# Kernel optimization log

Hardware: AMD Instinct MI355X
Metric: run time of the kernel (lower is better)

The kernel has to match this reference:

```python
import jax, jax.numpy as jnp
import numpy as np

B, N, K = 2, 16384, 16
C_IN, C_OUT, SHARE = 64, 64, 8
ATTN = C_OUT // SHARE  # 8
EPS = 1e-5


def bn(x, gamma, beta):
    # BatchNorm2d_P: normalize over (B, N, K) per channel, training-mode batch stats
    m = jnp.mean(x, axis=(0, 1, 2), keepdims=True)
    v = jnp.var(x, axis=(0, 1, 2), keepdims=True)  # biased variance
    return (x - m) * jax.lax.rsqrt(v + EPS) * gamma + beta


def gather(points, idx):
    # points: (B, N, C), idx: (B, N, K) -> (B, N, K, C)
    b, n, k = idx.shape
    flat = idx.reshape(b, n * k)
    out = jnp.take_along_axis(points, flat[:, :, None], axis=1)
    return out.reshape(b, n, k, points.shape[-1])


def setup_inputs() -> dict:
    key = jax.random.key(0)
    ks = jax.random.split(key, 16)
    w = lambda k_, shp: (jax.random.normal(k_, shp, dtype=jnp.float32) * 0.02)
    inp = {
        "xyz": jax.random.normal(ks[0], (B, N, 3), dtype=jnp.float32),
        "features": jax.random.normal(ks[1], (B, N, C_IN), dtype=jnp.float32),
        "knn_idx": jax.random.randint(ks[2], (B, N, K), 0, N),
        "Wq": w(ks[3], (C_IN, C_OUT)), "bq": jnp.zeros((C_OUT,), jnp.float32),
        "Wk": w(ks[4], (C_IN, C_OUT)), "bk": jnp.zeros((C_OUT,), jnp.float32),
        "Wv": w(ks[5], (C_IN, C_OUT)), "bv": jnp.zeros((C_OUT,), jnp.float32),
        "Wd1": w(ks[6], (3, 3)), "bd1": jnp.zeros((3,), jnp.float32),
        "gamma_d": jnp.ones((3,), jnp.float32), "beta_d": jnp.zeros((3,), jnp.float32),
        "Wd2": w(ks[7], (3, C_OUT)), "bd2": jnp.zeros((C_OUT,), jnp.float32),
        "gamma_g1": jnp.ones((C_OUT,), jnp.float32), "beta_g1": jnp.zeros((C_OUT,), jnp.float32),
        "Wg1": w(ks[8], (C_OUT, ATTN)), "bg1": jnp.zeros((ATTN,), jnp.float32),
        "gamma_g2": jnp.ones((ATTN,), jnp.float32), "beta_g2": jnp.zeros((ATTN,), jnp.float32),
        "Wg2": w(ks[9], (ATTN, ATTN)), "bg2": jnp.zeros((ATTN,), jnp.float32),
    }
    return inp


def reference(xyz, features, knn_idx, Wq, bq, Wk, bk, Wv, bv,
              Wd1, bd1, gamma_d, beta_d, Wd2, bd2,
              gamma_g1, beta_g1, Wg1, bg1, gamma_g2, beta_g2, Wg2, bg2):
    q = features @ Wq + bq                       # (B,N,C_OUT)
    k = gather(features @ Wk + bk, knn_idx)      # (B,N,K,C_OUT)
    v = gather(features @ Wv + bv, knn_idx)      # (B,N,K,C_OUT)
    knn_xyz = gather(xyz, knn_idx)               # (B,N,K,3)
    rel = xyz[:, :, None, :] - knn_xyz           # (B,N,K,3)
    # fc_delta: Linear(3,3) -> BN -> ReLU -> Linear(3,C_OUT)
    pos_enc = jax.nn.relu(bn(rel @ Wd1 + bd1, gamma_d, beta_d)) @ Wd2 + bd2  # (B,N,K,C_OUT)
    # einops.reduce 'b n k (i j) -> b n k j' with j=mid_planes is identity (i=1)
    attn_in = q[:, :, None, :] - k + pos_enc     # (B,N,K,C_OUT)
    # fc_gamma: BN -> ReLU -> Linear(C_OUT,ATTN) -> BN -> ReLU -> Linear(ATTN,ATTN)
    h = jax.nn.relu(bn(attn_in, gamma_g1, beta_g1)) @ Wg1 + bg1  # (B,N,K,ATTN)
    h = jax.nn.relu(bn(h, gamma_g2, beta_g2)) @ Wg2 + bg2        # (B,N,K,ATTN)
    attn = jax.nn.softmax(h, axis=2)             # softmax over K neighbors
    vp = (v + pos_enc).reshape(B, N, K, SHARE, ATTN)
    res = jnp.einsum('bnksa,bnka->bnsa', vp, attn)
    return res.reshape(B, N, C_OUT)
```

## Files before the change

### kernel.cpp

```cpp
#include <hip/hip_runtime.h>
#include <hip/hip_bf16.h>
#include <type_traits>

#define BB 2
#define NN 16384
#define KK 16
#define CC 64
#define AA 8
#define BN_PTS (BB*NN)
#define TOT (BB*NN*KK)
#define EPS 1e-5f

using bf = __hip_bfloat16;

__device__ __forceinline__ float b2f(bf x) { return __bfloat162float(x); }

template<typename T> __device__ __forceinline__ float ldt(const void* p, int i) {
    if constexpr (std::is_same<T, bf>::value) return b2f(((const bf*)p)[i]);
    else return ((const float*)p)[i];
}
template<typename T> __device__ __forceinline__ void stt(void* p, int i, float v) {
    if constexpr (std::is_same<T, bf>::value) ((bf*)p)[i] = __float2bfloat16(v);
    else ((float*)p)[i] = v;
}

__device__ __forceinline__ float waveReduce(float v) {
    #pragma unroll
    for (int off = 32; off; off >>= 1) v += __shfl_down(v, off, 64);
    return v;
}

__global__ void detect_kernel(const unsigned* __restrict__ gbits, int* __restrict__ flag) {
    if (threadIdx.x == 0 && blockIdx.x == 0)
        *flag = (gbits[0] == 0x3F803F80u) ? 1 : 0;
}

template<typename T>
__device__ void qkv_body(float* smem,
    const void* feat, const void* Wq, const void* bq, const void* Wk, const void* bk,
    const void* Wv, const void* bv, float* qf, bf* kfb, float* vf)
{
    float* fs = smem;
    const int which = threadIdx.x / 64;
    const int c = threadIdx.x & 63;
    const void* W    = (which == 0) ? Wq : (which == 1) ? Wk : Wv;
    const void* bias = (which == 0) ? bq : (which == 1) ? bk : bv;

    float w[64];
    #pragma unroll
    for (int j = 0; j < 64; j++) w[j] = ldt<T>(W, j*64 + c);
    const float bb_ = ldt<T>(bias, c);

    const int row0 = blockIdx.x * 32;
    for (int i = threadIdx.x; i < 32*64; i += 192)
        fs[i] = ldt<T>(feat, row0*64 + i);
    __syncthreads();

    for (int r = 0; r < 32; r++) {
        float acc = bb_;
        #pragma unroll
        for (int j = 0; j < 64; j++) acc = fmaf(fs[r*64 + j], w[j], acc);
        const int idx = (row0 + r)*64 + c;
        if (which == 1)      kfb[idx] = __float2bfloat16(acc);
        else if (which == 0) qf[idx] = acc;
        else                 vf[idx] = acc;
    }
}
__global__ __launch_bounds__(192) void qkv_kernel(
    const int* __restrict__ flag,
    const void* feat, const void* Wq, const void* bq, const void* Wk, const void* bk,
    const void* Wv, const void* bv, float* qf, bf* kfb, float* vf)
{
    extern __shared__ float smem[];
    if (*flag) qkv_body<bf>(smem, feat, Wq, bq, Wk, bk, Wv, bv, qf, kfb, vf);
    else       qkv_body<float>(smem, feat, Wq, bq, Wk, bk, Wv, bv, qf, kfb, vf);
}

template<typename T>
__device__ void statsd_body(float* smem,
    const void* xyz, const int* knn, const void* Wd1, const void* bd1,
    float* part, float* dx, float* dy, float* dz)
{
    float w[9], bi[3];
    #pragma unroll
    for (int i = 0; i < 9; i++) w[i] = ldt<T>(Wd1, i);
    #pragma unroll
    for (int i = 0; i < 3; i++) bi[i] = ldt<T>(bd1, i);

    float s[6] = {0,0,0,0,0,0};
    const int tid = blockIdx.x * 256 + threadIdx.x;
    for (int p = tid; p < TOT; p += 256*256) {
        const int bn = p >> 4;
        const int b  = bn >> 14;
        const int j  = knn[p];
        const int nb = (b << 14) + j;
        const float r0 = ldt<T>(xyz, bn*3+0) - ldt<T>(xyz, nb*3+0);
        const float r1 = ldt<T>(xyz, bn*3+1) - ldt<T>(xyz, nb*3+1);
        const float r2 = ldt<T>(xyz, bn*3+2) - ldt<T>(xyz, nb*3+2);
        const float d0 = fmaf(r0, w[0], fmaf(r1, w[3], fmaf(r2, w[6], bi[0])));
        const float d1 = fmaf(r0, w[1], fmaf(r1, w[4], fmaf(r2, w[7], bi[1])));
        const float d2 = fmaf(r0, w[2], fmaf(r1, w[5], fmaf(r2, w[8], bi[2])));
        if (dx) { dx[p] = d0; dy[p] = d1; dz[p] = d2; }
        s[0] += d0; s[1] += d1; s[2] += d2;
        s[3] = fmaf(d0, d0, s[3]); s[4] = fmaf(d1, d1, s[4]); s[5] = fmaf(d2, d2, s[5]);
    }
    float* red = smem;
    const int lane = threadIdx.x & 63, wave = threadIdx.x >> 6;
    #pragma unroll
    for (int i = 0; i < 6; i++) {
        const float r = waveReduce(s[i]);
        if (lane == 0) red[wave*6 + i] = r;
    }
    __syncthreads();
    if (threadIdx.x < 6)
        part[blockIdx.x*8 + threadIdx.x] =
            red[threadIdx.x] + red[6+threadIdx.x] + red[12+threadIdx.x] + red[18+threadIdx.x];
}
__global__ __launch_bounds__(256) void statsd_kernel(
    const int* __restrict__ flag,
    const void* xyz, const int* __restrict__ knn, const void* Wd1, const void* bd1,
    float* part, float* dx, float* dy, float* dz)
{
    extern __shared__ float smem[];
    if (*flag) statsd_body<bf>(smem, xyz, knn, Wd1, bd1, part, dx, dy, dz);
    else       statsd_body<float>(smem, xyz, knn, Wd1, bd1, part, dx, dy, dz);
}

template<typename T>
__device__ void finalize_d_body(float* sums,
    const float* part, const void* gamma, const void* beta, float* coef)
{
    const int t = threadIdx.x;
    if (t < 6) {
        float s = 0;
        for (int b = 0; b < 256; b++) s += part[b*8 + t];
        sums[t] = s;
    }
    __syncthreads();
    if (t < 3) {
        const float mean = sums[t] / (float)TOT;
        const float var  = sums[3+t] / (float)TOT - mean*mean;
        const float sc   = ldt<T>(gamma, t) * rsqrtf(var + EPS);
        coef[t]   = sc;
        coef[4+t] = ldt<T>(beta, t) - mean*sc;
    }
}
__global__ void finalize_d(const int* __restrict__ flag, const float* __restrict__ part,
                           const void* gamma, const void* beta, float* coef)
{
    extern __shared__ float smem[];
    if (*flag) finalize_d_body<bf>(smem, part, gamma, beta, coef);
    else       finalize_d_body<float>(smem, part, gamma, beta, coef);
}

template<typename T>
__device__ void statsg1_body(float* smem,
    const void* xyz, const int* knn, const float* qf, const bf* kfb,
    const void* Wd1, const void* bd1, const void* Wd2, const void* bd2,
    const float* coefd, float* part,
    const float* dx, const float* dy, const float* dz, bf* aibuf)
{
    const int lane = threadIdx.x & 63, wave = threadIdx.x >> 6;
    float w1[9], b1[3], sc[3], sh[3];
    #pragma unroll
    for (int i = 0; i < 9; i++) w1[i] = ldt<T>(Wd1, i);
    #pragma unroll
    for (int i = 0; i < 3; i++) { b1[i] = ldt<T>(bd1, i); sc[i] = coefd[i]; sh[i] = coefd[4+i]; }
    const float w2a = ldt<T>(Wd2, lane), w2b = ldt<T>(Wd2, 64+lane), w2c = ldt<T>(Wd2, 128+lane);
    const float bd2c = ldt<T>(bd2, lane);

    float sum = 0.f, sq = 0.f;
    for (int bn = blockIdx.x*4 + wave; bn < BN_PTS; bn += 2048*4) {
        const int b = bn >> 14;
        const float qv = qf[bn*64 + lane];
        float x0 = 0.f, x1 = 0.f, x2 = 0.f;
        if (!dx) { x0 = ldt<T>(xyz, bn*3+0); x1 = ldt<T>(xyz, bn*3+1); x2 = ldt<T>(xyz, bn*3+2); }
        #pragma unroll
        for (int k = 0; k < 16; k++) {
            const int it = bn*16 + k;
            const int j  = knn[it];
            const int nb = (b << 14) + j;
            float d0, d1, d2;
            if (dx) {
                d0 = dx[it]; d1 = dy[it]; d2 = dz[it];
            } else {
                const float r0 = x0 - ldt<T>(xyz, nb*3+0);
                const float r1 = x1 - ldt<T>(xyz, nb*3+1);
                const float r2 = x2 - ldt<T>(xyz, nb*3+2);
                d0 = fmaf(r0, w1[0], fmaf(r1, w1[3], fmaf(r2, w1[6], b1[0])));
                d1 = fmaf(r0, w1[1], fmaf(r1, w1[4], fmaf(r2, w1[7], b1[1])));
                d2 = fmaf(r0, w1[2], fmaf(r1, w1[5], fmaf(r2, w1[8], b1[2])));
            }
            d0 = fmaxf(fmaf(d0, sc[0], sh[0]), 0.f);
            d1 = fmaxf(fmaf(d1, sc[1], sh[1]), 0.f);
            d2 = fmaxf(fmaf(d2, sc[2], sh[2]), 0.f);
            const float pos = fmaf(d0, w2a, fmaf(d1, w2b, fmaf(d2, w2c, bd2c)));
            const float at = qv - b2f(kfb[nb*64 + lane]) + pos;
            if (aibuf) aibuf[(size_t)it*64 + lane] = __float2bfloat16(at);
            sum += at; sq = fmaf(at, at, sq);
        }
    }
    float* ls = smem;
    float* lq = smem + 256;
    ls[wave*64 + lane] = sum; lq[wave*64 + lane] = sq;
    __syncthreads();
    if (threadIdx.x < 64) {
        float a = 0.f, q = 0.f;
        #pragma unroll
        for (int w = 0; w < 4; w++) { a += ls[w*64 + lane]; q += lq[w*64 + lane]; }
        part[blockIdx.x*128 + lane]      = a;
        part[blockIdx.x*128 + 64 + lane] = q;
    }
}
__global__ __launch_bounds__(256) void statsg1_kernel(
    const int* __restrict__ flag,
    const void* xyz, const int* __restrict__ knn, const float* __restrict__ qf,
    const bf* __restrict__ kfb,
    const void* Wd1, const void* bd1, const void* Wd2, const void* bd2,
    const float* __restrict__ coefd, float* part,
    const float* dx, const float* dy, const float* dz, bf* aibuf)
{
    extern __shared__ float smem[];
    if (*flag) statsg1_body<bf>(smem, xyz, knn, qf, kfb, Wd1, bd1, Wd2, bd2, coefd, part, dx, dy, dz, aibuf);
    else       statsg1_body<float>(smem, xyz, knn, qf, kfb, Wd1, bd1, Wd2, bd2, coefd, part, dx, dy, dz, aibuf);
}

__global__ __launch_bounds__(256) void reduce_g1(const float* __restrict__ part,
                                                 float* __restrict__ partB)
{
    __shared__ float red[2][128];
    const int t = threadIdx.x;
    const int col = t & 127, chunk = t >> 7;
    const int r0 = blockIdx.x * 32;
    float s = 0.f;
    #pragma unroll
    for (int j = 0; j < 16; j++) s += part[(r0 + chunk + 2*j)*128 + col];
    red[chunk][col] = s;
    __syncthreads();
    if (t < 128) partB[blockIdx.x*128 + t] = red[0][t] + red[1][t];
}

template<typename T>
__device__ void finalize_g1_body(float* smem,
    const float* partB, const void* gamma, const void* beta, float* coef)
{
    float* red  = smem;
    float* sums = smem + 512;
    const int t = threadIdx.x;
    const int col = t & 127, chunk = t >> 7;
    float s = 0.f;
    #pragma unroll
    for (int j = 0; j < 16; j++) s += partB[(chunk + 4*j)*128 + col];
    red[chunk*128 + col] = s;
    __syncthreads();
    if (t < 128) sums[t] = red[t] + red[128+t] + red[256+t] + red[384+t];
    __syncthreads();
    if (t < 64) {
        const float mean = sums[t] / (float)TOT;
        const float var  = sums[64+t] / (float)TOT - mean*mean;
        const float sc   = ldt<T>(gamma, t) * rsqrtf(var + EPS);
        coef[t]    = sc;
        coef[64+t] = ldt<T>(beta, t) - mean*sc;
    }
}
__global__ __launch_bounds__(512) void finalize_g1(const int* __restrict__ flag,
    const float* __restrict__ partB, const void* gamma, const void* beta, float* coef)
{
    extern __shared__ float smem[];
    if (*flag) finalize_g1_body<bf>(smem, partB, gamma, beta, coef);
    else       finalize_g1_body<float>(smem, partB, gamma, beta, coef);
}

template<typename T>
__device__ void h1_fast_body(float* smem,
    const unsigned* aibuf, const float* coefg1, const void* Wg1, const void* bg1,
    float* h1, float* part)
{
    float* wg1s = smem;
    float* scs  = smem + 512;
    float* shs  = smem + 576;
    float* ssum = smem + 640;
    float* ssq  = smem + 672;
    const int t = threadIdx.x, lane = t & 63, wave = t >> 6;
    for (int i = t; i < 512; i += 256) wg1s[i] = ldt<T>(Wg1, i);
    if (t < 64) { scs[t] = coefg1[t]; shs[t] = coefg1[64 + t]; }
    __syncthreads();

    const size_t item = (size_t)blockIdx.x*256 + t;
    const uint4* src = (const uint4*)aibuf + item*8;
    float h[8];
    #pragma unroll
    for (int a = 0; a < 8; a++) h[a] = ldt<T>(bg1, a);
    #pragma unroll
    for (int cb = 0; cb < 8; cb++) {
        const uint4 u = src[cb];
        const unsigned uu[4] = {u.x, u.y, u.z, u.w};
        #pragma unroll
        for (int q = 0; q < 4; q++) {
            const int c0 = cb*8 + q*2;
            const float xlo = __uint_as_float(uu[q] << 16);
            const float xhi = __uint_as_float(uu[q] & 0xffff0000u);
            const float g0 = fmaxf(fmaf(xlo, scs[c0],   shs[c0]),   0.f);
            const float g1 = fmaxf(fmaf(xhi, scs[c0+1], shs[c0+1]), 0.f);
            #pragma unroll
            for (int a = 0; a < 8; a++) {
                h[a] = fmaf(g0, wg1s[c0*8 + a], h[a]);
                h[a] = fmaf(g1, wg1s[(c0+1)*8 + a], h[a]);
            }
        }
    }
    float4* hp = (float4*)(h1 + item*8);
    hp[0] = make_float4(h[0], h[1], h[2], h[3]);
    hp[1] = make_float4(h[4], h[5], h[6], h[7]);

    #pragma unroll
    for (int a = 0; a < 8; a++) {
        const float rs = waveReduce(h[a]);
        const float rq = waveReduce(h[a]*h[a]);
        if (lane == 0) { ssum[wave*8 + a] = rs; ssq[wave*8 + a] = rq; }
    }
    __syncthreads();
    if (t < 8) {
        part[blockIdx.x*16 + t]     = ssum[t] + ssum[8+t] + ssum[16+t] + ssum[24+t];
        part[blockIdx.x*16 + 8 + t] = ssq[t]  + ssq[8+t]  + ssq[16+t]  + ssq[24+t];
    }
}
__global__ __launch_bounds__(256) void h1_fast(const int* __restrict__ flag,
    const unsigned* __restrict__ aibuf, const float* __restrict__ coefg1,
    const void* Wg1, const void* bg1, float* h1, float* part)
{
    extern __shared__ float smem[];
    if (*flag) h1_fast_body<bf>(smem, aibuf, coefg1, Wg1, bg1, h1, part);
    else       h1_fast_body<float>(smem, aibuf, coefg1, Wg1, bg1, h1, part);
}

#define H1_PAD 68
template<typename T>
__device__ void h1_body(float* smem,
    const void* xyz, const int* knn, const float* qf, const bf* kfb,
    const void* Wd1, const void* bd1, const void* Wd2, const void* bd2,
    const float* coefd, const float* coefg1, const void* Wg1, const void* bg1,
    float* h1, float* part)
{
    float* xs   = smem;
    float* wg1s = smem + 8704;
    float* ssum = smem + 9216;
    float* ssq  = smem + 9248;
    const int t = threadIdx.x;
    const int lane = t & 63, wave = t >> 6;

    for (int i = t; i < 512; i += 256) wg1s[i] = ldt<T>(Wg1, i);

    float w1[9], b1[3], scd[3], shd[3];
    #pragma unroll
    for (int i = 0; i < 9; i++) w1[i] = ldt<T>(Wd1, i);
    #pragma unroll
    for (int i = 0; i < 3; i++) { b1[i] = ldt<T>(bd1, i); scd[i] = coefd[i]; shd[i] = coefd[4+i]; }
    const float w2a = ldt<T>(Wd2, lane), w2b = ldt<T>(Wd2, 64+lane), w2c = ldt<T>(Wd2, 128+lane);
    const float bd2c = ldt<T>(bd2, lane);
    const float sc1 = coefg1[lane], sh1 = coefg1[64+lane];
    const int lslot = (lane < 32) ? lane : lane + 4;

    #pragma unroll
    for (int g = 0; g < 2; g++) {
        const int pl = wave*2 + g;
        const int bn = blockIdx.x*8 + pl;
        const int b  = bn >> 14;
        const float qv = qf[bn*64 + lane];
        const float x0 = ldt<T>(xyz, bn*3+0), x1 = ldt<T>(xyz, bn*3+1), x2 = ldt<T>(xyz, bn*3+2);
        #pragma unroll
        for (int k = 0; k < 16; k++) {
            const int j  = knn[bn*16 + k];
            const int nb = (b << 14) + j;
            const float r0 = x0 - ldt<T>(xyz, nb*3+0);
            const float r1 = x1 - ldt<T>(xyz, nb*3+1);
            const float r2 = x2 - ldt<T>(xyz, nb*3+2);
            float d0 = fmaf(r0, w1[0], fmaf(r1, w1[3], fmaf(r2, w1[6], b1[0])));
            float d1 = fmaf(r0, w1[1], fmaf(r1, w1[4], fmaf(r2, w1[7], b1[1])));
            float d2 = fmaf(r0, w1[2], fmaf(r1, w1[5], fmaf(r2, w1[8], b1[2])));
            d0 = fmaxf(fmaf(d0, scd[0], shd[0]), 0.f);
            d1 = fmaxf(fmaf(d1, scd[1], shd[1]), 0.f);
            d2 = fmaxf(fmaf(d2, scd[2], shd[2]), 0.f);
            const float pos = fmaf(d0, w2a, fmaf(d1, w2b, fmaf(d2, w2c, bd2c)));
            const float at = qv - b2f(kfb[nb*64 + lane]) + pos;
            xs[(pl*16 + k)*H1_PAD + lslot] = fmaxf(fmaf(at, sc1, sh1), 0.f);
        }
    }
    __syncthreads();

    const int item = t >> 1;
    const int half = t & 1;
    float h[8];
    #pragma unroll
    for (int a = 0; a < 8; a++) h[a] = half ? 0.f : ldt<T>(bg1, a);
    const float4* xr = (const float4*)(xs + item*H1_PAD + half*36);
    const float* wbase = wg1s + half*256;
    #pragma unroll
    for (int cb = 0; cb < 8; cb++) {
        const float4 xv = xr[cb];
        #pragma unroll
        for (int jj = 0; jj < 4; jj++) {
            const float x = (jj == 0) ? xv.x : (jj == 1) ? xv.y : (jj == 2) ? xv.z : xv.w;
            const float4 wa = *(const float4*)&wbase[(cb*4 + jj)*8];
            const float4 wb = *(const float4*)&wbase[(cb*4 + jj)*8 + 4];
            h[0] = fmaf(x, wa.x, h[0]); h[1] = fmaf(x, wa.y, h[1]);
            h[2] = fmaf(x, wa.z, h[2]); h[3] = fmaf(x, wa.w, h[3]);
            h[4] = fmaf(x, wb.x, h[4]); h[5] = fmaf(x, wb.y, h[5]);
            h[6] = fmaf(x, wb.z, h[6]); h[7] = fmaf(x, wb.w, h[7]);
        }
    }
    #pragma unroll
    for (int a = 0; a < 8; a++) h[a] += __shfl_xor(h[a], 1, 64);

    const int it = blockIdx.x*128 + item;
    if (half == 0) {
        float4* hp = (float4*)(h1 + (size_t)it*8);
        hp[0] = make_float4(h[0], h[1], h[2], h[3]);
        hp[1] = make_float4(h[4], h[5], h[6], h[7]);
    }
    #pragma unroll
    for (int a = 0; a < 8; a++) {
        const float rs = waveReduce(h[a]);
        const float rq = waveReduce(h[a]*h[a]);
        if (lane == 0) { ssum[wave*8 + a] = 0.5f*rs; ssq[wave*8 + a] = 0.5f*rq; }
    }
    __syncthreads();
    if (t < 8) {
        part[blockIdx.x*16 + t]     = ssum[t] + ssum[8+t] + ssum[16+t] + ssum[24+t];
        part[blockIdx.x*16 + 8 + t] = ssq[t]  + ssq[8+t]  + ssq[16+t]  + ssq[24+t];
    }
}
__global__ __launch_bounds__(256, 4) void h1_kernel(const int* __restrict__ flag,
    const void* xyz, const int* __restrict__ knn, const float* __restrict__ qf,
    const bf* __restrict__ kfb,
    const void* Wd1, const void* bd1, const void* Wd2, const void* bd2,
    const float* __restrict__ coefd, const float* __restrict__ coefg1,
    const void* Wg1, const void* bg1, float* h1, float* part)
{
    extern __shared__ float smem[];
    if (*flag) h1_body<bf>(smem, xyz, knn, qf, kfb, Wd1, bd1, Wd2, bd2, coefd, coefg1, Wg1, bg1, h1, part);
    else       h1_body<float>(smem, xyz, knn, qf, kfb, Wd1, bd1, Wd2, bd2, coefd, coefg1, Wg1, bg1, h1, part);
}

__global__ __launch_bounds__(256) void reduce_g2(const float* __restrict__ part,
                                                 float* __restrict__ partB, int rows)
{
    __shared__ float red[16][16];
    const int t = threadIdx.x;
    const int col = t & 15, chunk = t >> 4;
    const int rpb = rows >> 6;
    const int r0 = blockIdx.x * rpb;
    float s = 0.f;
    for (int r = chunk; r < rpb; r += 16) s += part[(r0 + r)*16 + col];
    red[chunk][col] = s;
    __syncthreads();
    if (t < 16) {
        float a = 0.f;
        #pragma unroll
        for (int c = 0; c < 16; c++) a += red[c][t];
        partB[blockIdx.x*16 + t] = a;
    }
}

template<typename T>
__device__ void finalize_g2_body(float* smem,
    const float* partB, const void* gamma, const void* beta, float* coef)
{
    float* red  = smem;
    float* sums = smem + 256;
    const int t = threadIdx.x;
    const int col = t & 15, chunk = t >> 4;
    float s = 0.f;
    #pragma unroll
    for (int j = 0; j < 4; j++) s += partB[(chunk + 16*j)*16 + col];
    red[chunk*16 + col] = s;
    __syncthreads();
    if (t < 16) {
        float a = 0.f;
        #pragma unroll
        for (int c = 0; c < 16; c++) a += red[c*16 + t];
        sums[t] = a;
    }
    __syncthreads();
    if (t < 8) {
        const float mean = sums[t] / (float)TOT;
        const float var  = sums[8+t] / (float)TOT - mean*mean;
        const float sc   = ldt<T>(gamma, t) * rsqrtf(var + EPS);
        coef[t]   = sc;
        coef[8+t] = ldt<T>(beta, t) - mean*sc;
    }
}
__global__ __launch_bounds__(256) void finalize_g2(const int* __restrict__ flag,
    const float* __restrict__ partB, const void* gamma, const void* beta, float* coef)
{
    extern __shared__ float smem[];
    if (*flag) finalize_g2_body<bf>(smem, partB, gamma, beta, coef);
    else       finalize_g2_body<float>(smem, partB, gamma, beta, coef);
}

template<typename T>
__device__ void out_body(float* smem,
    const void* xyz, const int* knn, const float* vf, const float* h1,
    const void* Wd1, const void* bd1, const void* Wd2, const void* bd2,
    const float* coefd, const float* coefg2, const void* Wg2, const void* bg2,
    const float* dx, const float* dy, const float* dz, void* out)
{
    float* g   = smem;
    float* hh  = smem + 512;
    float* dd  = smem + 1024;
    float* wg2 = smem + 1216;
    int*  idxs = (int*)(smem + 1280);
    const int t = threadIdx.x;
    const int bn0 = blockIdx.x * 4;

    if (t < 64) wg2[t] = ldt<T>(Wg2, t);

    {
        const int p = t >> 6, f = t & 63;
        const int base = (bn0 + p) * 128;
        #pragma unroll
        for (int i = 0; i < 2; i++) {
            const int ff = f + i*64;
            const int a = ff & 7;
            const float v = h1[base + ff];
            g[p*128 + ff] = fmaxf(fmaf(v, coefg2[a], coefg2[8 + a]), 0.f);
        }
    }
    if (t < 64) {
        const int p = t >> 4, k = t & 15;
        const int bn = bn0 + p;
        const int b = bn >> 14;
        const int it = bn*16 + k;
        const int j = knn[it];
        idxs[p*16 + k] = j;
        float d0, d1, d2;
        if (dx) {
            d0 = dx[it]; d1 = dy[it]; d2 = dz[it];
        } else {
            const int nb = (b << 14) + j;
            const float r0 = ldt<T>(xyz, bn*3+0) - ldt<T>(xyz, nb*3+0);
            const float r1 = ldt<T>(xyz, bn*3+1) - ldt<T>(xyz, nb*3+1);
            const float r2 = ldt<T>(xyz, bn*3+2) - ldt<T>(xyz, nb*3+2);
            d0 = fmaf(r0, ldt<T>(Wd1,0), fmaf(r1, ldt<T>(Wd1,3), fmaf(r2, ldt<T>(Wd1,6), ldt<T>(bd1,0))));
            d1 = fmaf(r0, ldt<T>(Wd1,1), fmaf(r1, ldt<T>(Wd1,4), fmaf(r2, ldt<T>(Wd1,7), ldt<T>(bd1,1))));
            d2 = fmaf(r0, ldt<T>(Wd1,2), fmaf(r1, ldt<T>(Wd1,5), fmaf(r2, ldt<T>(Wd1,8), ldt<T>(bd1,2))));
        }
        dd[(p*16 + k)*3 + 0] = fmaxf(fmaf(d0, coefd[0], coefd[4]), 0.f);
        dd[(p*16 + k)*3 + 1] = fmaxf(fmaf(d1, coefd[1], coefd[5]), 0.f);
        dd[(p*16 + k)*3 + 2] = fmaxf(fmaf(d2, coefd[2], coefd[6]), 0.f);
    }
    __syncthreads();

    {
        #pragma unroll
        for (int i = 0; i < 2; i++) {
            const int o = t + i*256;
            const int p = o >> 7, f = o & 127;
            const int a = f & 7, k = f >> 3;
            float acc = ldt<T>(bg2, a);
            #pragma unroll
            for (int jj = 0; jj < 8; jj++) acc = fmaf(g[p*128 + k*8 + jj], wg2[jj*8 + a], acc);
            hh[p*128 + f] = acc;
        }
    }
    __syncthreads();

    if (t < 32) {
        const int p = t >> 3, a = t & 7;
        float m = -1e30f;
        #pragma unroll
        for (int k = 0; k < 16; k++) m = fmaxf(m, hh[p*128 + k*8 + a]);
        float e[16]; float s = 0.f;
        #pragma unroll
        for (int k = 0; k < 16; k++) { e[k] = __expf(hh[p*128 + k*8 + a] - m); s += e[k]; }
        const float inv = 1.f / s;
        #pragma unroll
        for (int k = 0; k < 16; k++) hh[p*128 + k*8 + a] = e[k] * inv;
    }
    __syncthreads();

    {
        const int p = t >> 6, c = t & 63, a = c & 7;
        const int bn = bn0 + p;
        const int b = bn >> 14;
        const float w0 = ldt<T>(Wd2, c), w1 = ldt<T>(Wd2, 64 + c), w2 = ldt<T>(Wd2, 128 + c);
        const float bd2c = ldt<T>(bd2, c);
        float acc = 0.f;
        #pragma unroll
        for (int k = 0; k < 16; k++) {
            const int j = idxs[p*16 + k];
            const float pos = fmaf(dd[(p*16+k)*3+0], w0, fmaf(dd[(p*16+k)*3+1], w1,
                              fmaf(dd[(p*16+k)*3+2], w2, bd2c)));
            const float vv = vf[((b << 14) + j)*64 + c] + pos;
            acc = fmaf(vv, hh[p*128 + k*8 + a], acc);
        }
        stt<T>(out, bn*64 + c, acc);
    }
}
__global__ __launch_bounds__(256) void out_kernel(const int* __restrict__ flag,
    const void* xyz, const int* __restrict__ knn, const float* __restrict__ vf,
    const float* __restrict__ h1,
    const void* Wd1, const void* bd1, const void* Wd2, const void* bd2,
    const float* __restrict__ coefd, const float* __restrict__ coefg2,
    const void* Wg2, const void* bg2,
    const float* dx, const float* dy, const float* dz, void* out)
{
    extern __shared__ float smem[];
    if (*flag) out_body<bf>(smem, xyz, knn, vf, h1, Wd1, bd1, Wd2, bd2, coefd, coefg2, Wg2, bg2, dx, dy, dz, out);
    else       out_body<float>(smem, xyz, knn, vf, h1, Wd1, bd1, Wd2, bd2, coefd, coefg2, Wg2, bg2, dx, dy, dz, out);
}

#define WS_BIG_FLOATS 28059808ull

extern "C" void kernel_launch(void* const* d_in, const int* in_sizes, int n_in,
                              void* d_out, int out_size, void* d_ws, size_t ws_size,
                              hipStream_t stream) {
    float* ws = (float*)d_ws;
    const void* xyz  = d_in[0];
    const void* feat = d_in[1];
    const int*  knn  = (const int*)d_in[2];
    const void *Wq = d_in[3], *bq = d_in[4], *Wk = d_in[5], *bk = d_in[6];
    const void *Wv = d_in[7], *bv = d_in[8], *Wd1 = d_in[9], *bd1 = d_in[10];
    const void *gd = d_in[11], *betad = d_in[12], *Wd2 = d_in[13], *bd2 = d_in[14];
    const void *gg1 = d_in[15], *bg1b = d_in[16], *Wg1 = d_in[17], *bg1 = d_in[18];
    const void *gg2 = d_in[19], *bg2b = d_in[20], *Wg2 = d_in[21], *bg2 = d_in[22];

    float* qf      = ws;
    bf*    kfb     = (bf*)(ws + 2097152);
    float* vf      = ws + 3145728;
    float* h1      = ws + 5242880;
    float* part_d  = ws + 9437184;
    float* partA   = ws + 9439232;
    float* partB   = ws + 9701376;
    float* coef_d  = ws + 9709568;
    float* coef_g1 = ws + 9709576;
    float* coef_g2 = ws + 9709704;
    int*   flag    = (int*)(ws + 9709720);
    const bool big = ws_size >= WS_BIG_FLOATS * 4ull;
    float* dx      = big ? ws + 9709728  : nullptr;
    float* dy      = big ? ws + 10234016 : nullptr;
    float* dz      = big ? ws + 10758304 : nullptr;
    bf*    aibuf   = big ? (bf*)(ws + 11282592) : nullptr;

    detect_kernel<<<1, 1, 0, stream>>>((const unsigned*)d_in[11], flag);
    qkv_kernel<<<1024, 192, 8192, stream>>>(flag, feat, Wq, bq, Wk, bk, Wv, bv, qf, kfb, vf);
    statsd_kernel<<<256, 256, 128, stream>>>(flag, xyz, knn, Wd1, bd1, part_d, dx, dy, dz);
    finalize_d<<<1, 64, 32, stream>>>(flag, part_d, gd, betad, coef_d);
    statsg1_kernel<<<2048, 256, 2048, stream>>>(flag, xyz, knn, qf, kfb, Wd1, bd1, Wd2, bd2,
                                                coef_d, partA, dx, dy, dz, aibuf);
    reduce_g1<<<64, 256, 0, stream>>>(partA, partB);
    finalize_g1<<<1, 512, 2560, stream>>>(flag, partB, gg1, bg1b, coef_g1);
    if (big) {
        h1_fast<<<2048, 256, 2816, stream>>>(flag, (const unsigned*)aibuf, coef_g1,
                                             Wg1, bg1, h1, partA);
        reduce_g2<<<64, 256, 0, stream>>>(partA, partB, 2048);
    } else {
        h1_kernel<<<4096, 256, 37120, stream>>>(flag, xyz, knn, qf, kfb, Wd1, bd1, Wd2, bd2,
                                                coef_d, coef_g1, Wg1, bg1, h1, partA);
        reduce_g2<<<64, 256, 0, stream>>>(partA, partB, 4096);
    }
    finalize_g2<<<1, 256, 1088, stream>>>(flag, partB, gg2, bg2b, coef_g2);
    out_kernel<<<8192, 256, 5376, stream>>>(flag, xyz, knn, vf, h1, Wd1, bd1, Wd2, bd2,
                                            coef_d, coef_g2, Wg2, bg2, dx, dy, dz, d_out);
}
```

Measured before the change: 270.7 us.

## Store V and h1 intermediates in bf16, widen out_kernel and statsd blocks

V projections and the h1 intermediate are now written as bf16 instead of fp32, which halves the bytes for the gathered V reads and the h1 round trip. out_kernel now handles 16 points per block instead of 4, so there are fewer blocks and more work per block. statsd drops its grid-stride loop and uses one element per thread across more blocks, and finalize_d reduces the larger partial array in parallel. Rounding V and h1 to bf16 adds precision error to the softmax logits and the output accumulation.

```diff
diff --git a/kernel.cpp b/kernel.cpp
--- a/kernel.cpp
+++ b/kernel.cpp
@@ -15,6 +15,16 @@
 
 __device__ __forceinline__ float b2f(bf x) { return __bfloat162float(x); }
 
+__device__ __forceinline__ unsigned short f2bu(float x) {
+    bf b = __float2bfloat16(x);
+    unsigned short u;
+    __builtin_memcpy(&u, &b, 2);
+    return u;
+}
+__device__ __forceinline__ unsigned packbf(float lo, float hi) {
+    return (unsigned)f2bu(lo) | ((unsigned)f2bu(hi) << 16);
+}
+
 template<typename T> __device__ __forceinline__ float ldt(const void* p, int i) {
     if constexpr (std::is_same<T, bf>::value) return b2f(((const bf*)p)[i]);
     else return ((const float*)p)[i];
@@ -38,7 +48,7 @@
 template<typename T>
 __device__ void qkv_body(float* smem,
     const void* feat, const void* Wq, const void* bq, const void* Wk, const void* bk,
-    const void* Wv, const void* bv, float* qf, bf* kfb, float* vf)
+    const void* Wv, const void* bv, float* qf, bf* kfb, bf* vfb)
 {
     float* fs = smem;
     const int which = threadIdx.x / 64;
@@ -61,19 +71,19 @@
         #pragma unroll
         for (int j = 0; j < 64; j++) acc = fmaf(fs[r*64 + j], w[j], acc);
         const int idx = (row0 + r)*64 + c;
-        if (which == 1)      kfb[idx] = __float2bfloat16(acc);
-        else if (which == 0) qf[idx] = acc;
-        else                 vf[idx] = acc;
+        if (which == 0)      qf[idx]  = acc;
+        else if (which == 1) kfb[idx] = __float2bfloat16(acc);
+        else                 vfb[idx] = __float2bfloat16(acc);
     }
 }
 __global__ __launch_bounds__(192) void qkv_kernel(
     const int* __restrict__ flag,
     const void* feat, const void* Wq, const void* bq, const void* Wk, const void* bk,
-    const void* Wv, const void* bv, float* qf, bf* kfb, float* vf)
-{
-    extern __shared__ float smem[];
-    if (*flag) qkv_body<bf>(smem, feat, Wq, bq, Wk, bk, Wv, bv, qf, kfb, vf);
-    else       qkv_body<float>(smem, feat, Wq, bq, Wk, bk, Wv, bv, qf, kfb, vf);
+    const void* Wv, const void* bv, float* qf, bf* kfb, bf* vfb)
+{
+    extern __shared__ float smem[];
+    if (*flag) qkv_body<bf>(smem, feat, Wq, bq, Wk, bk, Wv, bv, qf, kfb, vfb);
+    else       qkv_body<float>(smem, feat, Wq, bq, Wk, bk, Wv, bv, qf, kfb, vfb);
 }
 
 template<typename T>
@@ -87,23 +97,20 @@
     #pragma unroll
     for (int i = 0; i < 3; i++) bi[i] = ldt<T>(bd1, i);
 
-    float s[6] = {0,0,0,0,0,0};
-    const int tid = blockIdx.x * 256 + threadIdx.x;
-    for (int p = tid; p < TOT; p += 256*256) {
-        const int bn = p >> 4;
-        const int b  = bn >> 14;
-        const int j  = knn[p];
-        const int nb = (b << 14) + j;
-        const float r0 = ldt<T>(xyz, bn*3+0) - ldt<T>(xyz, nb*3+0);
-        const float r1 = ldt<T>(xyz, bn*3+1) - ldt<T>(xyz, nb*3+1);
-        const float r2 = ldt<T>(xyz, bn*3+2) - ldt<T>(xyz, nb*3+2);
-        const float d0 = fmaf(r0, w[0], fmaf(r1, w[3], fmaf(r2, w[6], bi[0])));
-        const float d1 = fmaf(r0, w[1], fmaf(r1, w[4], fmaf(r2, w[7], bi[1])));
-        const float d2 = fmaf(r0, w[2], fmaf(r1, w[5], fmaf(r2, w[8], bi[2])));
-        if (dx) { dx[p] = d0; dy[p] = d1; dz[p] = d2; }
-        s[0] += d0; s[1] += d1; s[2] += d2;
-        s[3] = fmaf(d0, d0, s[3]); s[4] = fmaf(d1, d1, s[4]); s[5] = fmaf(d2, d2, s[5]);
-    }
+    const int p = blockIdx.x * 256 + threadIdx.x;
+    const int bn = p >> 4;
+    const int b  = bn >> 14;
+    const int j  = knn[p];
+    const int nb = (b << 14) + j;
+    const float r0 = ldt<T>(xyz, bn*3+0) - ldt<T>(xyz, nb*3+0);
+    const float r1 = ldt<T>(xyz, bn*3+1) - ldt<T>(xyz, nb*3+1);
+    const float r2 = ldt<T>(xyz, bn*3+2) - ldt<T>(xyz, nb*3+2);
+    const float d0 = fmaf(r0, w[0], fmaf(r1, w[3], fmaf(r2, w[6], bi[0])));
+    const float d1 = fmaf(r0, w[1], fmaf(r1, w[4], fmaf(r2, w[7], bi[1])));
+    const float d2 = fmaf(r0, w[2], fmaf(r1, w[5], fmaf(r2, w[8], bi[2])));
+    if (dx) { dx[p] = d0; dy[p] = d1; dz[p] = d2; }
+    float s[6] = {d0, d1, d2, d0*d0, d1*d1, d2*d2};
+
     float* red = smem;
     const int lane = threadIdx.x & 63, wave = threadIdx.x >> 6;
     #pragma unroll
@@ -127,14 +134,22 @@
 }
 
 template<typename T>
-__device__ void finalize_d_body(float* sums,
+__device__ void finalize_d_body(float* smem,
     const float* part, const void* gamma, const void* beta, float* coef)
 {
+    float* red  = smem;
+    float* sums = smem + 256;
     const int t = threadIdx.x;
-    if (t < 6) {
-        float s = 0;
-        for (int b = 0; b < 256; b++) s += part[b*8 + t];
-        sums[t] = s;
+    const int col = t & 7, chunk = t >> 3;
+    float s = 0.f;
+    for (int r = chunk; r < 2048; r += 32) s += part[r*8 + col];
+    red[chunk*8 + col] = s;
+    __syncthreads();
+    if (t < 8) {
+        float a = 0.f;
+        #pragma unroll
+        for (int c = 0; c < 32; c++) a += red[c*8 + t];
+        sums[t] = a;
     }
     __syncthreads();
     if (t < 3) {
@@ -145,8 +160,8 @@
         coef[4+t] = ldt<T>(beta, t) - mean*sc;
     }
 }
-__global__ void finalize_d(const int* __restrict__ flag, const float* __restrict__ part,
-                           const void* gamma, const void* beta, float* coef)
+__global__ __launch_bounds__(256) void finalize_d(const int* __restrict__ flag,
+    const float* __restrict__ part, const void* gamma, const void* beta, float* coef)
 {
     extern __shared__ float smem[];
     if (*flag) finalize_d_body<bf>(smem, part, gamma, beta, coef);
@@ -274,7 +289,7 @@
 template<typename T>
 __device__ void h1_fast_body(float* smem,
     const unsigned* aibuf, const float* coefg1, const void* Wg1, const void* bg1,
-    float* h1, float* part)
+    unsigned* h1b, float* part)
 {
     float* wg1s = smem;
     float* scs  = smem + 512;
@@ -309,9 +324,10 @@
             }
         }
     }
-    float4* hp = (float4*)(h1 + item*8);
-    hp[0] = make_float4(h[0], h[1], h[2], h[3]);
-    hp[1] = make_float4(h[4], h[5], h[6], h[7]);
+    uint4 o4;
+    o4.x = packbf(h[0], h[1]); o4.y = packbf(h[2], h[3]);
+    o4.z = packbf(h[4], h[5]); o4.w = packbf(h[6], h[7]);
+    ((uint4*)h1b)[item] = o4;
 
     #pragma unroll
     for (int a = 0; a < 8; a++) {
@@ -327,11 +343,11 @@
 }
 __global__ __launch_bounds__(256) void h1_fast(const int* __restrict__ flag,
     const unsigned* __restrict__ aibuf, const float* __restrict__ coefg1,
-    const void* Wg1, const void* bg1, float* h1, float* part)
-{
-    extern __shared__ float smem[];
-    if (*flag) h1_fast_body<bf>(smem, aibuf, coefg1, Wg1, bg1, h1, part);
-    else       h1_fast_body<float>(smem, aibuf, coefg1, Wg1, bg1, h1, part);
+    const void* Wg1, const void* bg1, unsigned* h1b, float* part)
+{
+    extern __shared__ float smem[];
+    if (*flag) h1_fast_body<bf>(smem, aibuf, coefg1, Wg1, bg1, h1b, part);
+    else       h1_fast_body<float>(smem, aibuf, coefg1, Wg1, bg1, h1b, part);
 }
 
 #define H1_PAD 68
@@ -340,7 +356,7 @@
     const void* xyz, const int* knn, const float* qf, const bf* kfb,
     const void* Wd1, const void* bd1, const void* Wd2, const void* bd2,
     const float* coefd, const float* coefg1, const void* Wg1, const void* bg1,
-    float* h1, float* part)
+    unsigned* h1b, float* part)
 {
     float* xs   = smem;
     float* wg1s = smem + 8704;
@@ -414,9 +430,10 @@
 
     const int it = blockIdx.x*128 + item;
     if (half == 0) {
-        float4* hp = (float4*)(h1 + (size_t)it*8);
-        hp[0] = make_float4(h[0], h[1], h[2], h[3]);
-        hp[1] = make_float4(h[4], h[5], h[6], h[7]);
+        uint4 o4;
+        o4.x = packbf(h[0], h[1]); o4.y = packbf(h[2], h[3]);
+        o4.z = packbf(h[4], h[5]); o4.w = packbf(h[6], h[7]);
+        ((uint4*)h1b)[it] = o4;
     }
     #pragma unroll
     for (int a = 0; a < 8; a++) {
@@ -435,11 +452,11 @@
     const bf* __restrict__ kfb,
     const void* Wd1, const void* bd1, const void* Wd2, const void* bd2,
     const float* __restrict__ coefd, const float* __restrict__ coefg1,
-    const void* Wg1, const void* bg1, float* h1, float* part)
-{
-    extern __shared__ float smem[];
-    if (*flag) h1_body<bf>(smem, xyz, knn, qf, kfb, Wd1, bd1, Wd2, bd2, coefd, coefg1, Wg1, bg1, h1, part);
-    else       h1_body<float>(smem, xyz, knn, qf, kfb, Wd1, bd1, Wd2, bd2, coefd, coefg1, Wg1, bg1, h1, part);
+    const void* Wg1, const void* bg1, unsigned* h1b, float* part)
+{
+    extern __shared__ float smem[];
+    if (*flag) h1_body<bf>(smem, xyz, knn, qf, kfb, Wd1, bd1, Wd2, bd2, coefd, coefg1, Wg1, bg1, h1b, part);
+    else       h1_body<float>(smem, xyz, knn, qf, kfb, Wd1, bd1, Wd2, bd2, coefd, coefg1, Wg1, bg1, h1b, part);
 }
 
 __global__ __launch_bounds__(256) void reduce_g2(const float* __restrict__ part,
@@ -500,33 +517,36 @@
 
 template<typename T>
 __device__ void out_body(float* smem,
-    const void* xyz, const int* knn, const float* vf, const float* h1,
+    const void* xyz, const int* knn, const bf* vfb, const unsigned* h1b,
     const void* Wd1, const void* bd1, const void* Wd2, const void* bd2,
     const float* coefd, const float* coefg2, const void* Wg2, const void* bg2,
     const float* dx, const float* dy, const float* dz, void* out)
 {
     float* g   = smem;
-    float* hh  = smem + 512;
-    float* dd  = smem + 1024;
-    float* wg2 = smem + 1216;
-    int*  idxs = (int*)(smem + 1280);
+    float* hh  = smem + 2048;
+    float* dd  = smem + 4096;
+    float* wg2 = smem + 4864;
+    int*  idxs = (int*)(smem + 4928);
     const int t = threadIdx.x;
-    const int bn0 = blockIdx.x * 4;
+    const int bn0 = blockIdx.x * 16;
 
     if (t < 64) wg2[t] = ldt<T>(Wg2, t);
 
     {
-        const int p = t >> 6, f = t & 63;
-        const int base = (bn0 + p) * 128;
-        #pragma unroll
-        for (int i = 0; i < 2; i++) {
-            const int ff = f + i*64;
-            const int a = ff & 7;
-            const float v = h1[base + ff];
-            g[p*128 + ff] = fmaxf(fmaf(v, coefg2[a], coefg2[8 + a]), 0.f);
-        }
-    }
-    if (t < 64) {
+        const int p = t >> 4, q = t & 15;
+        const uint4 u = ((const uint4*)h1b)[(size_t)(bn0 + p)*16 + q];
+        const unsigned uu[4] = {u.x, u.y, u.z, u.w};
+        #pragma unroll
+        for (int w = 0; w < 4; w++) {
+            const int c0 = q*8 + w*2;
+            const int a = c0 & 7;
+            const float xlo = __uint_as_float(uu[w] << 16);
+            const float xhi = __uint_as_float(uu[w] & 0xffff0000u);
+            g[p*128 + c0]     = fmaxf(fmaf(xlo, coefg2[a],   coefg2[8+a]),   0.f);
+            g[p*128 + c0 + 1] = fmaxf(fmaf(xhi, coefg2[a+1], coefg2[9+a]),   0.f);
+        }
+    }
+    {
         const int p = t >> 4, k = t & 15;
         const int bn = bn0 + p;
         const int b = bn >> 14;
@@ -553,8 +573,8 @@
 
     {
         #pragma unroll
-        for (int i = 0; i < 2; i++) {
-            const int o = t + i*256;
+        for (int i = 0; i < 8; i++) {
+            const int o = i*256 + t;
             const int p = o >> 7, f = o & 127;
             const int a = f & 7, k = f >> 3;
             float acc = ldt<T>(bg2, a);
@@ -565,7 +585,7 @@
     }
     __syncthreads();
 
-    if (t < 32) {
+    if (t < 128) {
         const int p = t >> 3, a = t & 7;
         float m = -1e30f;
         #pragma unroll
@@ -580,37 +600,41 @@
     __syncthreads();
 
     {
-        const int p = t >> 6, c = t & 63, a = c & 7;
-        const int bn = bn0 + p;
-        const int b = bn >> 14;
-        const float w0 = ldt<T>(Wd2, c), w1 = ldt<T>(Wd2, 64 + c), w2 = ldt<T>(Wd2, 128 + c);
-        const float bd2c = ldt<T>(bd2, c);
-        float acc = 0.f;
-        #pragma unroll
-        for (int k = 0; k < 16; k++) {
-            const int j = idxs[p*16 + k];
-            const float pos = fmaf(dd[(p*16+k)*3+0], w0, fmaf(dd[(p*16+k)*3+1], w1,
-                              fmaf(dd[(p*16+k)*3+2], w2, bd2c)));
-            const float vv = vf[((b << 14) + j)*64 + c] + pos;
-            acc = fmaf(vv, hh[p*128 + k*8 + a], acc);
-        }
-        stt<T>(out, bn*64 + c, acc);
+        #pragma unroll
+        for (int i = 0; i < 4; i++) {
+            const int o = i*256 + t;
+            const int p = o >> 6, c = o & 63, a = c & 7;
+            const int bn = bn0 + p;
+            const int b = bn >> 14;
+            const float w0 = ldt<T>(Wd2, c), w1 = ldt<T>(Wd2, 64 + c), w2 = ldt<T>(Wd2, 128 + c);
+            const float bd2c = ldt<T>(bd2, c);
+            float acc = 0.f;
+            #pragma unroll
+            for (int k = 0; k < 16; k++) {
+                const int j = idxs[p*16 + k];
+                const float pos = fmaf(dd[(p*16+k)*3+0], w0, fmaf(dd[(p*16+k)*3+1], w1,
+                                  fmaf(dd[(p*16+k)*3+2], w2, bd2c)));
+                const float vv = b2f(vfb[((b << 14) + j)*64 + c]) + pos;
+                acc = fmaf(vv, hh[p*128 + k*8 + a], acc);
+            }
+            stt<T>(out, bn*64 + c, acc);
+        }
     }
 }
 __global__ __launch_bounds__(256) void out_kernel(const int* __restrict__ flag,
-    const void* xyz, const int* __restrict__ knn, const float* __restrict__ vf,
-    const float* __restrict__ h1,
+    const void* xyz, const int* __restrict__ knn, const bf* __restrict__ vfb,
+    const unsigned* __restrict__ h1b,
     const void* Wd1, const void* bd1, const void* Wd2, const void* bd2,
     const float* __restrict__ coefd, const float* __restrict__ coefg2,
     const void* Wg2, const void* bg2,
     const float* dx, const float* dy, const float* dz, void* out)
 {
     extern __shared__ float smem[];
-    if (*flag) out_body<bf>(smem, xyz, knn, vf, h1, Wd1, bd1, Wd2, bd2, coefd, coefg2, Wg2, bg2, dx, dy, dz, out);
-    else       out_body<float>(smem, xyz, knn, vf, h1, Wd1, bd1, Wd2, bd2, coefd, coefg2, Wg2, bg2, dx, dy, dz, out);
-}
-
-#define WS_BIG_FLOATS 28059808ull
+    if (*flag) out_body<bf>(smem, xyz, knn, vfb, h1b, Wd1, bd1, Wd2, bd2, coefd, coefg2, Wg2, bg2, dx, dy, dz, out);
+    else       out_body<float>(smem, xyz, knn, vfb, h1b, Wd1, bd1, Wd2, bd2, coefd, coefg2, Wg2, bg2, dx, dy, dz, out);
+}
+
+#define WS_BIG_FLOATS 24928416ull
 
 extern "C" void kernel_launch(void* const* d_in, const int* in_sizes, int n_in,
                               void* d_out, int out_size, void* d_ws, size_t ws_size,
@@ -625,41 +649,41 @@
     const void *gg1 = d_in[15], *bg1b = d_in[16], *Wg1 = d_in[17], *bg1 = d_in[18];
     const void *gg2 = d_in[19], *bg2b = d_in[20], *Wg2 = d_in[21], *bg2 = d_in[22];
 
-    float* qf      = ws;
-    bf*    kfb     = (bf*)(ws + 2097152);
-    float* vf      = ws + 3145728;
-    float* h1      = ws + 5242880;
-    float* part_d  = ws + 9437184;
-    float* partA   = ws + 9439232;
-    float* partB   = ws + 9701376;
-    float* coef_d  = ws + 9709568;
-    float* coef_g1 = ws + 9709576;
-    float* coef_g2 = ws + 9709704;
-    int*   flag    = (int*)(ws + 9709720);
+    float*    qf      = ws;
+    bf*       kfb     = (bf*)(ws + 2097152);
+    bf*       vfb     = (bf*)(ws + 3145728);
+    unsigned* h1b     = (unsigned*)(ws + 4194304);
+    float*    part_d  = ws + 6291456;
+    float*    partA   = ws + 6307840;
+    float*    partB   = ws + 6569984;
+    float*    coef_d  = ws + 6578176;
+    float*    coef_g1 = ws + 6578184;
+    float*    coef_g2 = ws + 6578312;
+    int*      flag    = (int*)(ws + 6578328);
     const bool big = ws_size >= WS_BIG_FLOATS * 4ull;
-    float* dx      = big ? ws + 9709728  : nullptr;
-    float* dy      = big ? ws + 10234016 : nullptr;
-    float* dz      = big ? ws + 10758304 : nullptr;
-    bf*    aibuf   = big ? (bf*)(ws + 11282592) : nullptr;
+    float* dx    = big ? ws + 6578336 : nullptr;
+    float* dy    = big ? ws + 7102624 : nullptr;
+    float* dz    = big ? ws + 7626912 : nullptr;
+    bf*    aibuf = big ? (bf*)(ws + 8151200) : nullptr;
 
     detect_kernel<<<1, 1, 0, stream>>>((const unsigned*)d_in[11], flag);
-    qkv_kernel<<<1024, 192, 8192, stream>>>(flag, feat, Wq, bq, Wk, bk, Wv, bv, qf, kfb, vf);
-    statsd_kernel<<<256, 256, 128, stream>>>(flag, xyz, knn, Wd1, bd1, part_d, dx, dy, dz);
-    finalize_d<<<1, 64, 32, stream>>>(flag, part_d, gd, betad, coef_d);
+    qkv_kernel<<<1024, 192, 8192, stream>>>(flag, feat, Wq, bq, Wk, bk, Wv, bv, qf, kfb, vfb);
+    statsd_kernel<<<2048, 256, 96, stream>>>(flag, xyz, knn, Wd1, bd1, part_d, dx, dy, dz);
+    finalize_d<<<1, 256, 1056, stream>>>(flag, part_d, gd, betad, coef_d);
     statsg1_kernel<<<2048, 256, 2048, stream>>>(flag, xyz, knn, qf, kfb, Wd1, bd1, Wd2, bd2,
                                                 coef_d, partA, dx, dy, dz, aibuf);
     reduce_g1<<<64, 256, 0, stream>>>(partA, partB);
     finalize_g1<<<1, 512, 2560, stream>>>(flag, partB, gg1, bg1b, coef_g1);
     if (big) {
         h1_fast<<<2048, 256, 2816, stream>>>(flag, (const unsigned*)aibuf, coef_g1,
-                                             Wg1, bg1, h1, partA);
+                                             Wg1, bg1, h1b, partA);
         reduce_g2<<<64, 256, 0, stream>>>(partA, partB, 2048);
     } else {
         h1_kernel<<<4096, 256, 37120, stream>>>(flag, xyz, knn, qf, kfb, Wd1, bd1, Wd2, bd2,
-                                                coef_d, coef_g1, Wg1, bg1, h1, partA);
+                                                coef_d, coef_g1, Wg1, bg1, h1b, partA);
         reduce_g2<<<64, 256, 0, stream>>>(partA, partB, 4096);
     }
     finalize_g2<<<1, 256, 1088, stream>>>(flag, partB, gg2, bg2b, coef_g2);
-    out_kernel<<<8192, 256, 5376, stream>>>(flag, xyz, knn, vf, h1, Wd1, bd1, Wd2, bd2,
-                                            coef_d, coef_g2, Wg2, bg2, dx, dy, dz, d_out);
-}
+    out_kernel<<<2048, 256, 20736, stream>>>(flag, xyz, knn, vfb, h1b, Wd1, bd1, Wd2, bd2,
+                                             coef_d, coef_g2, Wg2, bg2, dx, dy, dz, d_out);
+}
```

New measurement: 278.9 us. 3.0% more time.
